# Optimization experiments

Hardware: AMD Instinct MI355X
Metric: run time of the kernel (lower is better)

Reference implementation:

```python
import jax, jax.numpy as jnp
from jax import lax
import numpy as np

V, E, H = 27, 64, 128
B, S_ENC, S_DEC = 256, 512, 512


def _simple_rnn(x_emb, Wx, Wh, b, h0):
    """Keras SimpleRNN: h_t = tanh(x_t @ Wx + h_{t-1} @ Wh + b).
    x_emb: [B, S, E]; returns (outputs [B, S, H], last state [B, H])."""
    # Precompute input projections for all timesteps (one big GEMM).
    xw = jnp.einsum('bse,eh->bsh', x_emb, Wx) + b  # [B, S, H]

    def step(h, xw_t):
        h = jnp.tanh(xw_t + h @ Wh)
        return h, h

    h_last, hs = lax.scan(step, h0, jnp.swapaxes(xw, 0, 1))  # scan over time
    return jnp.swapaxes(hs, 0, 1), h_last


def setup_inputs() -> dict:
    key = jax.random.key(0)
    ks = jax.random.split(key, 8)
    s = lambda fan_in: 1.0 / np.sqrt(fan_in)
    return {
        'enc_ids': jax.random.randint(ks[0], (B, S_ENC), 0, V, dtype=jnp.int32),
        'dec_ids': jax.random.randint(ks[1], (B, S_DEC), 0, V, dtype=jnp.int32),
        'embed':  jax.random.normal(ks[2], (V, E), jnp.float32) * 0.05,
        'enc_Wx': jax.random.normal(ks[3], (E, H), jnp.float32) * s(E),
        'enc_Wh': jax.random.normal(ks[4], (H, H), jnp.float32) * s(H),
        'enc_b':  jnp.zeros((H,), jnp.float32),
        'dec_Wx': jax.random.normal(ks[5], (E, H), jnp.float32) * s(E),
        'dec_Wh': jax.random.normal(ks[6], (H, H), jnp.float32) * s(H),
        'dec_b':  jnp.zeros((H,), jnp.float32),
        'dense_W': jax.random.normal(ks[7], (H, V), jnp.float32) * s(H),
        'dense_b': jnp.zeros((V,), jnp.float32),
    }


def reference(enc_ids, dec_ids, embed, enc_Wx, enc_Wh, enc_b,
              dec_Wx, dec_Wh, dec_b, dense_W, dense_b):
    enc_emb = embed[enc_ids]                      # [B, S_enc, E]
    h0 = jnp.zeros((enc_ids.shape[0], H), embed.dtype)
    _, enc_state = _simple_rnn(enc_emb, enc_Wx, enc_Wh, enc_b, h0)
    dec_emb = embed[dec_ids]                      # [B, S_dec, E]
    dec_out, _ = _simple_rnn(dec_emb, dec_Wx, dec_Wh, dec_b, enc_state)
    logits = jnp.einsum('bsh,hv->bsv', dec_out, dense_W) + dense_b
    return logits
```

## Files before the change

kernel.cpp:

```cpp
#include <hip/hip_runtime.h>

#define V_ 27
#define E_ 64
#define H_ 128
#define S_ 512

typedef float f32x4 __attribute__((ext_vector_type(4)));

#define BAR() asm volatile("s_waitcnt lgkmcnt(0)\n\ts_barrier" ::: "memory")

#define PINW() asm volatile("" : "+v"(R0), "+v"(R1), "+v"(R2), "+v"(R3), \
                                 "+v"(R4), "+v"(R5), "+v"(R6), "+v"(R7))
#define PIND() asm volatile("" : "+v"(D0), "+v"(D1))

template<int CTRL>
__device__ __forceinline__ float dpp_add(float x) {
    int y = __builtin_amdgcn_update_dpp(0, __builtin_bit_cast(int, x), CTRL, 0xF, 0xF, true);
    return x + __builtin_bit_cast(float, y);
}
#define QP_1032 0xB1
#define QP_2301 0x4E
#define RR8 0x128
#define RR4 0x124
#define RR2 0x122
#define RR1 0x121

__device__ __forceinline__ float fast_tanhf(float z) {
    float e = __expf(2.0f * z);
    return 1.0f - __fdividef(2.0f, e + 1.0f);
}

__device__ __forceinline__ float dot8(f32x4 a, f32x4 b, f32x4 wa, f32x4 wb) {
    float p = a.x * wa.x;
    p = fmaf(a.y, wa.y, p); p = fmaf(a.z, wa.z, p); p = fmaf(a.w, wa.w, p);
    p = fmaf(b.x, wb.x, p); p = fmaf(b.y, wb.y, p); p = fmaf(b.z, wb.z, p);
    p = fmaf(b.w, wb.w, p);
    return p;
}

__global__ void prep_T(const float* __restrict__ embed,
                       const float* __restrict__ eWx, const float* __restrict__ eb,
                       const float* __restrict__ dWx, const float* __restrict__ db_,
                       float* __restrict__ Tg) {
    int tbl = blockIdx.x / V_;
    int v   = blockIdx.x - tbl * V_;
    int j   = threadIdx.x;
    const float* Wx = tbl ? dWx : eWx;
    const float* bb = tbl ? db_ : eb;
    float s = bb[j];
    #pragma unroll
    for (int e = 0; e < E_; ++e) s = fmaf(embed[v * E_ + e], Wx[e * H_ + j], s);
    Tg[tbl * V_ * H_ + v * H_ + j] = s;
}

#define ACC4(HV, R) \
    p0 = fmaf((HV), (R).x, p0); p1 = fmaf((HV), (R).y, p1); \
    p2 = fmaf((HV), (R).z, p2); p3 = fmaf((HV), (R).w, p3)

#define RNN_STEP(HSRC, HDST, DENSEF, LOADPAIRF, IDP, TGB, DOSTORE, OUTP) do {       \
    PINW();                                                                         \
    if (DENSEF) PIND();                                                             \
    int2 idpr_n = idpr;                                                             \
    if (LOADPAIRF) idpr_n = *(const int2*)((IDP) + 2);      \
    float Tv_n = (TGB)[id_next * H_ + jdiag];              \
    const f32x4* hbp = (const f32x4*)((HSRC) + 12 * kk);                            \
    f32x4 ha = hbp[0], hc = hbp[1];                            \
    float p0 = 0.f, p1 = 0.f, p2 = 0.f, p3 = 0.f;                                   \
    ACC4(ha.x, R0); ACC4(ha.y, R1); ACC4(ha.z, R2); ACC4(ha.w, R3);                 \
    ACC4(hc.x, R4); ACC4(hc.y, R5); ACC4(hc.z, R6); ACC4(hc.w, R7);                 \
    p0 = dpp_add<QP_2301>(dpp_add<QP_1032>(p0));                                    \
    p1 = dpp_add<QP_2301>(dpp_add<QP_1032>(p1));                                    \
    p2 = dpp_add<QP_2301>(dpp_add<QP_1032>(p2));                                    \
    p3 = dpp_add<QP_2301>(dpp_add<QP_1032>(p3));                                    \
    float s01 = c1 ? p1 : p0;                                                       \
    float s23 = c1 ? p3 : p2;                                                       \
    float r   = c2 ? s23 : s01;                                                     \
    r = dpp_add<RR8>(r);                                                            \
    r = dpp_add<RR4>(r);                                                            \
    float hnew = fast_tanhf(r + Tv);                                                \
    if (wrlane) (HDST)[wrword] = hnew;                      \
    if (DENSEF) {                                                                   \
        float d = dot8(ha, hc, D0, D1);                                             \
        d = dpp_add<RR1>(dpp_add<RR2>(dpp_add<RR4>(dpp_add<RR8>(d))));              \
        if (DOSTORE) (OUTP)[0] = d + db;                   \
    }                                                                               \
    BAR();                                                                          \
    if (LOADPAIRF) { idpr = idpr_n; id_next = idpr_n.x; }                           \
    else           { id_next = idpr.y; }                                            \
    Tv = Tv_n;                                                                      \
} while (0)

__global__ __attribute__((amdgpu_flat_work_group_size(512, 512), amdgpu_waves_per_eu(2, 2)))
void seq2seq_rnn_kernel(const int* __restrict__ enc_ids, const int* __restrict__ dec_ids,
                        const float* __restrict__ enc_Wh, const float* __restrict__ dec_Wh,
                        const float* __restrict__ dense_W, const float* __restrict__ dense_b,
                        const float* __restrict__ Tg,
                        float* __restrict__ out) {
    __shared__ __align__(16) float lds_h0[192];
    __shared__ __align__(16) float lds_h1[192];
    __shared__ __align__(16) int   lds_ids[2 * S_ + 2];

    const int tid  = threadIdx.x;
    const int b    = blockIdx.x;
    const int lane = tid & 63;
    const int w    = tid >> 6;
    const int jl   = lane >> 4;
    const int kk   = lane & 15;
    const int j0     = (w << 4) + (jl << 2);
    const int jdiag  = j0 + (lane & 3);
    const int wrword = 12 * (jdiag >> 3) + (jdiag & 7);
    const bool wrlane = (kk < 4);
    const bool c1 = (lane & 1) != 0;
    const bool c2 = (lane & 2) != 0;
    const int vd   = (w << 2) | jl;

    if (tid < 256) ((int2*)lds_ids)[tid] = ((const int2*)(enc_ids + b * S_))[tid];
    else ((int2*)(lds_ids + S_))[tid - 256] = ((const int2*)(dec_ids + b * S_))[tid - 256];
    if (tid < 2) lds_ids[2 * S_ + tid] = 0;
    if (tid < 192) lds_h0[tid] = 0.0f;

    f32x4 R0, R1, R2, R3, R4, R5, R6, R7;
    {
        const float* wp = enc_Wh + (8 * kk) * H_ + j0;
        R0 = *(const f32x4*)(wp + 0 * H_); R1 = *(const f32x4*)(wp + 1 * H_);
        R2 = *(const f32x4*)(wp + 2 * H_); R3 = *(const f32x4*)(wp + 3 * H_);
        R4 = *(const f32x4*)(wp + 4 * H_); R5 = *(const f32x4*)(wp + 5 * H_);
        R6 = *(const f32x4*)(wp + 6 * H_); R7 = *(const f32x4*)(wp + 7 * H_);
    }

    f32x4 D0, D1; float db = 0.0f;
    {
        int vc = (vd < V_) ? vd : 0;
        const float* dp = dense_W + (8 * kk) * V_ + vc;
        D0.x = dp[0 * V_]; D0.y = dp[1 * V_]; D0.z = dp[2 * V_]; D0.w = dp[3 * V_];
        D1.x = dp[4 * V_]; D1.y = dp[5 * V_]; D1.z = dp[6 * V_]; D1.w = dp[7 * V_];
        if (vd < V_) db = dense_b[vd];
    }
    const bool dlane = (kk == 0) && (vd < V_);
    float* outd = out + b * (S_ * V_) + vd;
    __syncthreads();

    {
        int2  idpr = make_int2(0, 0);
        int   id_next = lds_ids[1];
        float Tv      = Tg[lds_ids[0] * H_ + jdiag];
        for (int t = 0; t < S_; t += 2) {
            RNN_STEP(lds_h0, lds_h1, false, true,  lds_ids + t, Tg, false, (float*)out);
            RNN_STEP(lds_h1, lds_h0, false, false, lds_ids + t, Tg, false, (float*)out);
        }
    }

    {
        const float* wp = dec_Wh + (8 * kk) * H_ + j0;
        R0 = *(const f32x4*)(wp + 0 * H_); R1 = *(const f32x4*)(wp + 1 * H_);
        R2 = *(const f32x4*)(wp + 2 * H_); R3 = *(const f32x4*)(wp + 3 * H_);
        R4 = *(const f32x4*)(wp + 4 * H_); R5 = *(const f32x4*)(wp + 5 * H_);
        R6 = *(const f32x4*)(wp + 6 * H_); R7 = *(const f32x4*)(wp + 7 * H_);
    }

    {
        const int*   ids_d = lds_ids + S_;
        const float* Td    = Tg + V_ * H_;
        int2  idpr = make_int2(0, 0);
        int   id_next = ids_d[1];
        float Tv      = Td[ids_d[0] * H_ + jdiag];
        for (int t = 0; t < S_; t += 2) {
            RNN_STEP(lds_h0, lds_h1, true, true,  ids_d + t, Td,
                     dlane && (t > 0), outd + (t - 1) * V_);
            RNN_STEP(lds_h1, lds_h0, true, false, ids_d + t, Td,
                     dlane, outd + t * V_);
        }
    }

    {
        const f32x4* hbp = (const f32x4*)(lds_h0 + 12 * kk);
        f32x4 ha = hbp[0], hc = hbp[1];
        float d = dot8(ha, hc, D0, D1);
        d = dpp_add<RR1>(dpp_add<RR2>(dpp_add<RR4>(dpp_add<RR8>(d))));
        if (dlane) outd[(S_ - 1) * V_] = d + db;
    }
}

extern "C" void kernel_launch(void* const* d_in, const int* in_sizes, int n_in,
                              void* d_out, int out_size, void* d_ws, size_t ws_size,
                              hipStream_t stream) {
    const int*   enc_ids = (const int*)d_in[0];
    const int*   dec_ids = (const int*)d_in[1];
    const float* embed   = (const float*)d_in[2];
    const float* enc_Wx  = (const float*)d_in[3];
    const float* enc_Wh  = (const float*)d_in[4];
    const float* enc_b   = (const float*)d_in[5];
    const float* dec_Wx  = (const float*)d_in[6];
    const float* dec_Wh  = (const float*)d_in[7];
    const float* dec_b   = (const float*)d_in[8];
    const float* dense_W = (const float*)d_in[9];
    const float* dense_b = (const float*)d_in[10];
    float* out = (float*)d_out;
    float* Tg  = (float*)d_ws;

    hipLaunchKernelGGL(prep_T, dim3(2 * V_), dim3(H_), 0, stream,
                       embed, enc_Wx, enc_b, dec_Wx, dec_b, Tg);
    hipLaunchKernelGGL(seq2seq_rnn_kernel, dim3(256), dim3(512), 0, stream,
                       enc_ids, dec_ids, enc_Wh, dec_Wh, dense_W, dense_b, Tg, out);
}
```

Baseline: 412.0 us.

## Halve RNN workgroup to 4 waves with 16-deep per-lane K slices

Reorganizes the recurrent step so each lane holds a 16-row slice of Wh (16 f32x4 registers) instead of 8, which lets the workgroup shrink from 8 waves to 4. The k-reduction needs one fewer cross-lane DPP stage and the h vector is padded to a 20-float stride in LDS. The lane-to-(j,k) mapping is reshuffled, and the dense-head reduction changes to match. Fewer waves should make each per-step barrier cheaper, at the cost of roughly double the FMA work per lane and higher register pressure.

```diff
diff --git a/kernel.cpp b/kernel.cpp
--- a/kernel.cpp
+++ b/kernel.cpp
@@ -9,9 +9,11 @@
 
 #define BAR() asm volatile("s_waitcnt lgkmcnt(0)\n\ts_barrier" ::: "memory")
 
-#define PINW() asm volatile("" : "+v"(R0), "+v"(R1), "+v"(R2), "+v"(R3), \
-                                 "+v"(R4), "+v"(R5), "+v"(R6), "+v"(R7))
-#define PIND() asm volatile("" : "+v"(D0), "+v"(D1))
+#define PINW() asm volatile("" : "+v"(R0), "+v"(R1), "+v"(R2), "+v"(R3),   \
+                                 "+v"(R4), "+v"(R5), "+v"(R6), "+v"(R7),   \
+                                 "+v"(R8), "+v"(R9), "+v"(R10), "+v"(R11), \
+                                 "+v"(R12), "+v"(R13), "+v"(R14), "+v"(R15))
+#define PIND() asm volatile("" : "+v"(D0), "+v"(D1), "+v"(D2), "+v"(D3))
 
 template<int CTRL>
 __device__ __forceinline__ float dpp_add(float x) {
@@ -21,20 +23,19 @@
 #define QP_1032 0xB1
 #define QP_2301 0x4E
 #define RR8 0x128
-#define RR4 0x124
-#define RR2 0x122
-#define RR1 0x121
 
 __device__ __forceinline__ float fast_tanhf(float z) {
     float e = __expf(2.0f * z);
     return 1.0f - __fdividef(2.0f, e + 1.0f);
 }
 
-__device__ __forceinline__ float dot8(f32x4 a, f32x4 b, f32x4 wa, f32x4 wb) {
+__device__ __forceinline__ float dot16(f32x4 a, f32x4 b, f32x4 c, f32x4 d,
+                                       f32x4 wa, f32x4 wb, f32x4 wc, f32x4 wd) {
     float p = a.x * wa.x;
     p = fmaf(a.y, wa.y, p); p = fmaf(a.z, wa.z, p); p = fmaf(a.w, wa.w, p);
-    p = fmaf(b.x, wb.x, p); p = fmaf(b.y, wb.y, p); p = fmaf(b.z, wb.z, p);
-    p = fmaf(b.w, wb.w, p);
+    p = fmaf(b.x, wb.x, p); p = fmaf(b.y, wb.y, p); p = fmaf(b.z, wb.z, p); p = fmaf(b.w, wb.w, p);
+    p = fmaf(c.x, wc.x, p); p = fmaf(c.y, wc.y, p); p = fmaf(c.z, wc.z, p); p = fmaf(c.w, wc.w, p);
+    p = fmaf(d.x, wd.x, p); p = fmaf(d.y, wd.y, p); p = fmaf(d.z, wd.z, p); p = fmaf(d.w, wd.w, p);
     return p;
 }
 
@@ -62,12 +63,14 @@
     if (DENSEF) PIND();                                                             \
     int2 idpr_n = idpr;                                                             \
     if (LOADPAIRF) idpr_n = *(const int2*)((IDP) + 2);      \
-    float Tv_n = (TGB)[id_next * H_ + jdiag];              \
-    const f32x4* hbp = (const f32x4*)((HSRC) + 12 * kk);                            \
-    f32x4 ha = hbp[0], hc = hbp[1];                            \
+    float Tv_n = (TGB)[id_next * H_ + jd];                 \
+    const f32x4* hbp = (const f32x4*)((HSRC) + 20 * kk);                            \
+    f32x4 ha = hbp[0], hb = hbp[1], hc = hbp[2], hd = hbp[3];  \
     float p0 = 0.f, p1 = 0.f, p2 = 0.f, p3 = 0.f;                                   \
-    ACC4(ha.x, R0); ACC4(ha.y, R1); ACC4(ha.z, R2); ACC4(ha.w, R3);                 \
-    ACC4(hc.x, R4); ACC4(hc.y, R5); ACC4(hc.z, R6); ACC4(hc.w, R7);                 \
+    ACC4(ha.x, R0);  ACC4(ha.y, R1);  ACC4(ha.z, R2);  ACC4(ha.w, R3);              \
+    ACC4(hb.x, R4);  ACC4(hb.y, R5);  ACC4(hb.z, R6);  ACC4(hb.w, R7);              \
+    ACC4(hc.x, R8);  ACC4(hc.y, R9);  ACC4(hc.z, R10); ACC4(hc.w, R11);             \
+    ACC4(hd.x, R12); ACC4(hd.y, R13); ACC4(hd.z, R14); ACC4(hd.w, R15);             \
     p0 = dpp_add<QP_2301>(dpp_add<QP_1032>(p0));                                    \
     p1 = dpp_add<QP_2301>(dpp_add<QP_1032>(p1));                                    \
     p2 = dpp_add<QP_2301>(dpp_add<QP_1032>(p2));                                    \
@@ -75,13 +78,12 @@
     float s01 = c1 ? p1 : p0;                                                       \
     float s23 = c1 ? p3 : p2;                                                       \
     float r   = c2 ? s23 : s01;                                                     \
-    r = dpp_add<RR8>(r);                                                            \
-    r = dpp_add<RR4>(r);                                                            \
+    r = dpp_add<RR8>(r);                                        \
     float hnew = fast_tanhf(r + Tv);                                                \
     if (wrlane) (HDST)[wrword] = hnew;                      \
     if (DENSEF) {                                                                   \
-        float d = dot8(ha, hc, D0, D1);                                             \
-        d = dpp_add<RR1>(dpp_add<RR2>(dpp_add<RR4>(dpp_add<RR8>(d))));              \
+        float d = dot16(ha, hb, hc, hd, D0, D1, D2, D3);                            \
+        d = dpp_add<RR8>(dpp_add<QP_2301>(dpp_add<QP_1032>(d)));                    \
         if (DOSTORE) (OUTP)[0] = d + db;                   \
     }                                                                               \
     BAR();                                                                          \
@@ -90,60 +92,66 @@
     Tv = Tv_n;                                                                      \
 } while (0)
 
-__global__ __attribute__((amdgpu_flat_work_group_size(512, 512), amdgpu_waves_per_eu(2, 2)))
+__global__ __attribute__((amdgpu_flat_work_group_size(256, 256), amdgpu_waves_per_eu(2, 2)))
 void seq2seq_rnn_kernel(const int* __restrict__ enc_ids, const int* __restrict__ dec_ids,
                         const float* __restrict__ enc_Wh, const float* __restrict__ dec_Wh,
                         const float* __restrict__ dense_W, const float* __restrict__ dense_b,
                         const float* __restrict__ Tg,
                         float* __restrict__ out) {
-    __shared__ __align__(16) float lds_h0[192];
-    __shared__ __align__(16) float lds_h1[192];
+    __shared__ __align__(16) float lds_h0[160];
+    __shared__ __align__(16) float lds_h1[160];
     __shared__ __align__(16) int   lds_ids[2 * S_ + 2];
 
     const int tid  = threadIdx.x;
     const int b    = blockIdx.x;
     const int lane = tid & 63;
     const int w    = tid >> 6;
-    const int jl   = lane >> 4;
-    const int kk   = lane & 15;
-    const int j0     = (w << 4) + (jl << 2);
-    const int jdiag  = j0 + (lane & 3);
-    const int wrword = 12 * (jdiag >> 3) + (jdiag & 7);
-    const bool wrlane = (kk < 4);
+    const int kk   = (lane & 3) | (((lane >> 3) & 1) << 2);
+    const int jl   = ((lane >> 2) & 1) | (((lane >> 4) & 3) << 1);
+    const int j0     = (w << 5) + (jl << 2);
+    const int jd     = j0 + (lane & 3);
+    const int wrword = 20 * (jd >> 4) + (jd & 15);
+    const bool wrlane = (lane & 8) == 0;
     const bool c1 = (lane & 1) != 0;
     const bool c2 = (lane & 2) != 0;
-    const int vd   = (w << 2) | jl;
-
-    if (tid < 256) ((int2*)lds_ids)[tid] = ((const int2*)(enc_ids + b * S_))[tid];
-    else ((int2*)(lds_ids + S_))[tid - 256] = ((const int2*)(dec_ids + b * S_))[tid - 256];
+    const int vd   = (w << 3) | jl;
+
+    if (tid < 128) ((int4*)lds_ids)[tid] = ((const int4*)(enc_ids + b * S_))[tid];
+    else ((int4*)(lds_ids + S_))[tid - 128] = ((const int4*)(dec_ids + b * S_))[tid - 128];
     if (tid < 2) lds_ids[2 * S_ + tid] = 0;
-    if (tid < 192) lds_h0[tid] = 0.0f;
-
-    f32x4 R0, R1, R2, R3, R4, R5, R6, R7;
-    {
-        const float* wp = enc_Wh + (8 * kk) * H_ + j0;
-        R0 = *(const f32x4*)(wp + 0 * H_); R1 = *(const f32x4*)(wp + 1 * H_);
-        R2 = *(const f32x4*)(wp + 2 * H_); R3 = *(const f32x4*)(wp + 3 * H_);
-        R4 = *(const f32x4*)(wp + 4 * H_); R5 = *(const f32x4*)(wp + 5 * H_);
-        R6 = *(const f32x4*)(wp + 6 * H_); R7 = *(const f32x4*)(wp + 7 * H_);
-    }
-
-    f32x4 D0, D1; float db = 0.0f;
+    if (tid < 160) lds_h0[tid] = 0.0f;
+
+    f32x4 R0, R1, R2, R3, R4, R5, R6, R7, R8, R9, R10, R11, R12, R13, R14, R15;
+    {
+        const float* wp = enc_Wh + (16 * kk) * H_ + j0;
+        R0  = *(const f32x4*)(wp +  0 * H_); R1  = *(const f32x4*)(wp +  1 * H_);
+        R2  = *(const f32x4*)(wp +  2 * H_); R3  = *(const f32x4*)(wp +  3 * H_);
+        R4  = *(const f32x4*)(wp +  4 * H_); R5  = *(const f32x4*)(wp +  5 * H_);
+        R6  = *(const f32x4*)(wp +  6 * H_); R7  = *(const f32x4*)(wp +  7 * H_);
+        R8  = *(const f32x4*)(wp +  8 * H_); R9  = *(const f32x4*)(wp +  9 * H_);
+        R10 = *(const f32x4*)(wp + 10 * H_); R11 = *(const f32x4*)(wp + 11 * H_);
+        R12 = *(const f32x4*)(wp + 12 * H_); R13 = *(const f32x4*)(wp + 13 * H_);
+        R14 = *(const f32x4*)(wp + 14 * H_); R15 = *(const f32x4*)(wp + 15 * H_);
+    }
+
+    f32x4 D0, D1, D2, D3; float db = 0.0f;
     {
         int vc = (vd < V_) ? vd : 0;
-        const float* dp = dense_W + (8 * kk) * V_ + vc;
-        D0.x = dp[0 * V_]; D0.y = dp[1 * V_]; D0.z = dp[2 * V_]; D0.w = dp[3 * V_];
-        D1.x = dp[4 * V_]; D1.y = dp[5 * V_]; D1.z = dp[6 * V_]; D1.w = dp[7 * V_];
+        const float* dp = dense_W + (16 * kk) * V_ + vc;
+        D0.x = dp[ 0 * V_]; D0.y = dp[ 1 * V_]; D0.z = dp[ 2 * V_]; D0.w = dp[ 3 * V_];
+        D1.x = dp[ 4 * V_]; D1.y = dp[ 5 * V_]; D1.z = dp[ 6 * V_]; D1.w = dp[ 7 * V_];
+        D2.x = dp[ 8 * V_]; D2.y = dp[ 9 * V_]; D2.z = dp[10 * V_]; D2.w = dp[11 * V_];
+        D3.x = dp[12 * V_]; D3.y = dp[13 * V_]; D3.z = dp[14 * V_]; D3.w = dp[15 * V_];
         if (vd < V_) db = dense_b[vd];
     }
-    const bool dlane = (kk == 0) && (vd < V_);
+    const bool dlane = ((lane & 11) == 0) && (vd < V_);
     float* outd = out + b * (S_ * V_) + vd;
     __syncthreads();
 
     {
         int2  idpr = make_int2(0, 0);
         int   id_next = lds_ids[1];
-        float Tv      = Tg[lds_ids[0] * H_ + jdiag];
+        float Tv      = Tg[lds_ids[0] * H_ + jd];
         for (int t = 0; t < S_; t += 2) {
             RNN_STEP(lds_h0, lds_h1, false, true,  lds_ids + t, Tg, false, (float*)out);
             RNN_STEP(lds_h1, lds_h0, false, false, lds_ids + t, Tg, false, (float*)out);
@@ -151,11 +159,15 @@
     }
 
     {
-        const float* wp = dec_Wh + (8 * kk) * H_ + j0;
-        R0 = *(const f32x4*)(wp + 0 * H_); R1 = *(const f32x4*)(wp + 1 * H_);
-        R2 = *(const f32x4*)(wp + 2 * H_); R3 = *(const f32x4*)(wp + 3 * H_);
-        R4 = *(const f32x4*)(wp + 4 * H_); R5 = *(const f32x4*)(wp + 5 * H_);
-        R6 = *(const f32x4*)(wp + 6 * H_); R7 = *(const f32x4*)(wp + 7 * H_);
+        const float* wp = dec_Wh + (16 * kk) * H_ + j0;
+        R0  = *(const f32x4*)(wp +  0 * H_); R1  = *(const f32x4*)(wp +  1 * H_);
+        R2  = *(const f32x4*)(wp +  2 * H_); R3  = *(const f32x4*)(wp +  3 * H_);
+        R4  = *(const f32x4*)(wp +  4 * H_); R5  = *(const f32x4*)(wp +  5 * H_);
+        R6  = *(const f32x4*)(wp +  6 * H_); R7  = *(const f32x4*)(wp +  7 * H_);
+        R8  = *(const f32x4*)(wp +  8 * H_); R9  = *(const f32x4*)(wp +  9 * H_);
+        R10 = *(const f32x4*)(wp + 10 * H_); R11 = *(const f32x4*)(wp + 11 * H_);
+        R12 = *(const f32x4*)(wp + 12 * H_); R13 = *(const f32x4*)(wp + 13 * H_);
+        R14 = *(const f32x4*)(wp + 14 * H_); R15 = *(const f32x4*)(wp + 15 * H_);
     }
 
     {
@@ -163,7 +175,7 @@
         const float* Td    = Tg + V_ * H_;
         int2  idpr = make_int2(0, 0);
         int   id_next = ids_d[1];
-        float Tv      = Td[ids_d[0] * H_ + jdiag];
+        float Tv      = Td[ids_d[0] * H_ + jd];
         for (int t = 0; t < S_; t += 2) {
             RNN_STEP(lds_h0, lds_h1, true, true,  ids_d + t, Td,
                      dlane && (t > 0), outd + (t - 1) * V_);
@@ -173,10 +185,10 @@
     }
 
     {
-        const f32x4* hbp = (const f32x4*)(lds_h0 + 12 * kk);
-        f32x4 ha = hbp[0], hc = hbp[1];
-        float d = dot8(ha, hc, D0, D1);
-        d = dpp_add<RR1>(dpp_add<RR2>(dpp_add<RR4>(dpp_add<RR8>(d))));
+        const f32x4* hbp = (const f32x4*)(lds_h0 + 20 * kk);
+        f32x4 ha = hbp[0], hb = hbp[1], hc = hbp[2], hd = hbp[3];
+        float d = dot16(ha, hb, hc, hd, D0, D1, D2, D3);
+        d = dpp_add<RR8>(dpp_add<QP_2301>(dpp_add<QP_1032>(d)));
         if (dlane) outd[(S_ - 1) * V_] = d + db;
     }
 }
@@ -200,6 +212,6 @@
 
     hipLaunchKernelGGL(prep_T, dim3(2 * V_), dim3(H_), 0, stream,
                        embed, enc_Wx, enc_b, dec_Wx, dec_b, Tg);
-    hipLaunchKernelGGL(seq2seq_rnn_kernel, dim3(256), dim3(512), 0, stream,
+    hipLaunchKernelGGL(seq2seq_rnn_kernel, dim3(256), dim3(256), 0, stream,
                        enc_ids, dec_ids, enc_Wh, dec_Wh, dense_W, dense_b, Tg, out);
 }
```

After: 413.3 us. Within noise of the previous version (+0.3%).
